# Kernel tuning notes

Hardware: AMD Instinct MI355X
Metric: run time of the kernel (lower is better)

## Reference

```python
import jax, jax.numpy as jnp
import numpy as np

N, H, W, C = 2, 96, 96, 256
HEADS, P = 8, 25
DH = C // HEADS
HID = int(C * 4.0)


def _ln(x, g, b):
    m = jnp.mean(x, axis=-1, keepdims=True)
    v = jnp.var(x, axis=-1, keepdims=True)
    return (x - m) / jnp.sqrt(v + 1e-5) * g + b


def _deform_sample(value, loc, h, w):
    # value: (n, heads, h*w, dh); loc: (n, Lq, heads, P, 2) normalized to [0,1] (x,y)
    # Bilinear sampling with align_corners=False and zero padding, as in
    # grid_sample used by MSDeformAttn.
    n = value.shape[0]
    gx = loc[..., 0] * w - 0.5
    gy = loc[..., 1] * h - 0.5
    x0 = jnp.floor(gx)
    y0 = jnp.floor(gy)
    fx = gx - x0
    fy = gy - y0
    out = jnp.zeros((n, HEADS, gx.shape[1] * P, DH), dtype=value.dtype)
    for dx, dy in ((0, 0), (1, 0), (0, 1), (1, 1)):
        xi = x0 + dx
        yi = y0 + dy
        wgt = (fx if dx else 1.0 - fx) * (fy if dy else 1.0 - fy)
        valid = ((xi >= 0) & (xi <= w - 1) & (yi >= 0) & (yi <= h - 1)).astype(value.dtype)
        xi_c = jnp.clip(xi, 0, w - 1).astype(jnp.int32)
        yi_c = jnp.clip(yi, 0, h - 1).astype(jnp.int32)
        idx = yi_c * w + xi_c                                   # (n, Lq, heads, P)
        idx = jnp.transpose(idx, (0, 2, 1, 3)).reshape(n, HEADS, -1)
        g = jnp.take_along_axis(value, idx[..., None], axis=2)  # (n, heads, Lq*P, dh)
        wv = jnp.transpose(wgt * valid, (0, 2, 1, 3)).reshape(n, HEADS, -1, 1)
        out = out + g * wv
    return out


def setup_inputs() -> dict:
    key = jax.random.key(0)
    ks = jax.random.split(key, 20)
    s = 0.02
    inp = {
        'x': jax.random.normal(ks[0], (N, H, W, C), jnp.float32),
        'ref_points': jax.random.uniform(ks[1], (N, H * W, 1, 2), jnp.float32),
        'spatial_shapes': jnp.array([[H, W]], dtype=jnp.int32),
        'level_start_index': jnp.zeros((1,), dtype=jnp.int32),
        'ln1_g': jnp.ones((C,), jnp.float32),
        'ln1_b': jnp.zeros((C,), jnp.float32),
        'w_off': jax.random.normal(ks[2], (C, HEADS * P * 2), jnp.float32) * s,
        'b_off': jax.random.normal(ks[3], (HEADS * P * 2,), jnp.float32) * s,
        'w_attn': jax.random.normal(ks[4], (C, HEADS * P), jnp.float32) * s,
        'b_attn': jax.random.normal(ks[5], (HEADS * P,), jnp.float32) * s,
        'w_val': jax.random.normal(ks[6], (C, C), jnp.float32) * s,
        'b_val': jnp.zeros((C,), jnp.float32),
        'w_out': jax.random.normal(ks[7], (C, C), jnp.float32) * s,
        'b_out': jnp.zeros((C,), jnp.float32),
        'ln2_g': jnp.ones((C,), jnp.float32),
        'ln2_b': jnp.zeros((C,), jnp.float32),
        'w_fc1': jax.random.normal(ks[8], (C, HID), jnp.float32) * s,
        'b_fc1': jnp.zeros((HID,), jnp.float32),
        'w_fc2': jax.random.normal(ks[9], (HID, C), jnp.float32) * s,
        'b_fc2': jnp.zeros((C,), jnp.float32),
    }
    return inp


def reference(x, ref_points, spatial_shapes, level_start_index,
              ln1_g, ln1_b, w_off, b_off, w_attn, b_attn,
              w_val, b_val, w_out, b_out, ln2_g, ln2_b,
              w_fc1, b_fc1, w_fc2, b_fc2):
    n, h, w, c = x.shape
    lq = h * w
    shortcut = x
    # pre-norm + flatten to query
    q = _ln(x, ln1_g, ln1_b).reshape(n, lq, c)
    # MSDeformAttn (n_levels = 1)
    value = (q @ w_val + b_val).reshape(n, lq, HEADS, DH).transpose(0, 2, 1, 3)
    off = (q @ w_off + b_off).reshape(n, lq, HEADS, P, 2)
    aw = jax.nn.softmax((q @ w_attn + b_attn).reshape(n, lq, HEADS, P), axis=-1)
    norm = jnp.array([w, h], dtype=x.dtype)          # offsets normalized by (W, H)
    ref = ref_points[:, :, 0, :]                     # (n, Lq, 2)
    loc = ref[:, :, None, None, :] + off / norm      # (n, Lq, heads, P, 2)
    sampled = _deform_sample(value, loc, h, w).reshape(n, HEADS, lq, P, DH)
    attn = jnp.einsum('nqhp,nhqpd->nqhd', aw, sampled).reshape(n, lq, c)
    attn = attn @ w_out + b_out
    x1 = shortcut + attn.reshape(n, h, w, c)
    # MLP block
    y = _ln(x1, ln2_g, ln2_b)
    y = jax.nn.gelu(y @ w_fc1 + b_fc1, approximate=False) @ w_fc2 + b_fc2
    return x1 + y
```

## Files before the change

kernel.cpp:

```cpp
#include <hip/hip_runtime.h>
#include <hip/hip_bf16.h>
#include <math.h>

typedef __hip_bfloat16 bf16;
typedef __attribute__((ext_vector_type(8))) short short8;
typedef __attribute__((ext_vector_type(4))) float f32x4;

#define NB 2
#define HH 96
#define WW 96
#define CC 256
#define NHEADS 8
#define PP 25
#define DHH 32
#define HIDN 1024
#define LQ (HH*WW)
#define TT (NB*LQ)
#define NVC 896
#define TB 8

__device__ __forceinline__ float b2f(bf16 v){ return __bfloat162float(v); }
__device__ __forceinline__ bf16  f2b(float v){ return __float2bfloat16(v); }
__device__ __forceinline__ float lo_bf(unsigned u){ return __uint_as_float(u << 16); }
__device__ __forceinline__ float hi_bf(unsigned u){ return __uint_as_float(u & 0xffff0000u); }

__device__ __forceinline__ void gl2lds16(const void* g, void* l) {
    __builtin_amdgcn_global_load_lds(
        (const __attribute__((address_space(1))) unsigned int*)g,
        (__attribute__((address_space(3))) unsigned int*)l, 16, 0, 0);
}

__global__ __launch_bounds__(256) void prep_all(const float* __restrict__ w_val,
                                                const float* __restrict__ w_off,
                                                const float* __restrict__ w_attn,
                                                const float* __restrict__ w_fc1,
                                                const float* __restrict__ w_fc2,
                                                const float* __restrict__ w_out,
                                                const float* __restrict__ b_val,
                                                const float* __restrict__ b_off,
                                                const float* __restrict__ b_attn,
                                                bf16* __restrict__ wvcT,
                                                bf16* __restrict__ wfc1T,
                                                bf16* __restrict__ wfc2T,
                                                bf16* __restrict__ woutT,
                                                float* __restrict__ bvc)
{
    const int idx = blockIdx.x*256 + threadIdx.x;
    if (idx < 229376) {
        int n = idx >> 8, k = idx & 255;
        float v = (n < 256) ? w_val[(size_t)k*256 + n]
                : (n < 656) ? w_off[(size_t)k*400 + (n-256)]
                : (n < 856) ? w_attn[(size_t)k*200 + (n-656)] : 0.f;
        wvcT[idx] = f2b(v);
    } else if (idx < 491520) {
        int j = idx - 229376; int n = j >> 8, k = j & 255;
        wfc1T[j] = f2b(w_fc1[(size_t)k*1024 + n]);
    } else if (idx < 753664) {
        int j = idx - 491520; int n = j >> 10, k = j & 1023;
        wfc2T[j] = f2b(w_fc2[(size_t)k*256 + n]);
    } else if (idx < 819200) {
        int j = idx - 753664; int n = j >> 8, k = j & 255;
        woutT[j] = f2b(w_out[(size_t)k*256 + n]);
    }
    if (idx < NVC)
        bvc[idx] = (idx < 256) ? b_val[idx]
                 : (idx < 656) ? b_off[idx-256]
                 : (idx < 856) ? b_attn[idx-656] : 0.f;
}

__global__ __launch_bounds__(256) void ln_kernel(const float* __restrict__ x,
                                                 const float* __restrict__ g,
                                                 const float* __restrict__ b,
                                                 bf16* __restrict__ out)
{
    const int t = blockIdx.x*4 + (threadIdx.x >> 6);
    const int l = threadIdx.x & 63;
    const float4 v = *(const float4*)(x + (size_t)t*CC + l*4);
    float s  = v.x + v.y + v.z + v.w;
    float s2 = v.x*v.x + v.y*v.y + v.z*v.z + v.w*v.w;
    #pragma unroll
    for (int m = 1; m < 64; m <<= 1) { s += __shfl_xor(s, m); s2 += __shfl_xor(s2, m); }
    const float mean = s * (1.f/CC);
    const float var  = s2 * (1.f/CC) - mean*mean;
    const float rs   = 1.f / sqrtf(var + 1e-5f);
    const float4 gg = *(const float4*)(g + l*4);
    const float4 bb = *(const float4*)(b + l*4);
    bf16 o[4];
    o[0] = f2b((v.x-mean)*rs*gg.x + bb.x);
    o[1] = f2b((v.y-mean)*rs*gg.y + bb.y);
    o[2] = f2b((v.z-mean)*rs*gg.z + bb.z);
    o[3] = f2b((v.w-mean)*rs*gg.w + bb.w);
    *(uint2*)(out + (size_t)t*CC + l*4) = *(uint2*)o;
}

template<int EPI, int K, int N>
__global__ __launch_bounds__(256) void mfma_gemm(const bf16* __restrict__ A,
                                                 const bf16* __restrict__ Bt,
                                                 const float* __restrict__ bias,
                                                 void* __restrict__ outv,
                                                 const float* __restrict__ resid)
{
    __shared__ short As[128*64];
    __shared__ short Bs[128*64];
    const int tid = threadIdx.x;
    const int w = tid >> 6, l = tid & 63;
    const int bm = blockIdx.x, bn = blockIdx.y;

    const bf16* sbase[8];
    short*      lbase[8];
    {
        const int lrow = l >> 3;
        const int q    = (l & 7) ^ lrow;
        #pragma unroll
        for (int j = 0; j < 8; j++) {
            int r = w*8 + j;
            bool isA = r < 16;
            int rr = isA ? r : r - 16;
            int row = rr*8 + lrow;
            size_t grow = (size_t)((isA ? bm : bn)*128 + row);
            sbase[j] = (isA ? A : Bt) + grow*K + q*8;
            lbase[j] = (isA ? As : Bs) + rr*512;
        }
    }

    int aoff[2][4], boff[2][4];
    #pragma unroll
    for (int s = 0; s < 2; s++)
        #pragma unroll
        for (int i = 0; i < 4; i++) {
            int q = s*4 + (l >> 4);
            int m = 64*(w >> 1) + i*16 + (l & 15);
            int n = 64*(w &  1) + i*16 + (l & 15);
            aoff[s][i] = (m*8 + (q ^ (m & 7))) * 8;
            boff[s][i] = (n*8 + (q ^ (n & 7))) * 8;
        }

    f32x4 acc[4][4];
    #pragma unroll
    for (int i = 0; i < 4; i++)
        #pragma unroll
        for (int j = 0; j < 4; j++)
            acc[i][j] = (f32x4){0.f, 0.f, 0.f, 0.f};

    for (int k0 = 0; k0 < K; k0 += 64) {
        #pragma unroll
        for (int j = 0; j < 8; j++)
            gl2lds16(sbase[j] + k0, lbase[j]);
        __syncthreads();
        #pragma unroll
        for (int s = 0; s < 2; s++) {
            short8 af[4], bfr[4];
            #pragma unroll
            for (int i = 0; i < 4; i++) {
                af[i]  = *(const short8*)(As + aoff[s][i]);
                bfr[i] = *(const short8*)(Bs + boff[s][i]);
            }
            #pragma unroll
            for (int i = 0; i < 4; i++)
                #pragma unroll
                for (int j = 0; j < 4; j++)
                    acc[i][j] = __builtin_amdgcn_mfma_f32_16x16x32_bf16(af[i], bfr[j], acc[i][j], 0, 0, 0);
        }
        __syncthreads();
    }

    const int row0 = bm*128 + 64*(w >> 1) + (l >> 4)*4;
    const int col0 = bn*128 + 64*(w &  1) + (l & 15);
    #pragma unroll
    for (int i = 0; i < 4; i++) {
        #pragma unroll
        for (int j = 0; j < 4; j++) {
            const int col = col0 + j*16;
            const float bs = bias[col];
            #pragma unroll
            for (int r = 0; r < 4; r++) {
                const int row = row0 + i*16 + r;
                float v = acc[i][j][r] + bs;
                size_t o = (size_t)row * N + col;
                if (EPI == 0) {
                    ((bf16*)outv)[o] = f2b(v);
                } else if (EPI == 2) {
                    ((bf16*)outv)[o] = f2b(0.5f * v * (1.f + erff(v * 0.70710678118654752f)));
                } else {
                    ((float*)outv)[o] = v + resid[o];
                }
            }
        }
    }
}

struct __align__(16) Tap { _Float16 w[4]; unsigned short i[4]; };

__global__ __launch_bounds__(256) void sample_kernel(const bf16* __restrict__ vc,
                                                     const float* __restrict__ refp,
                                                     bf16* __restrict__ samp)
{
    __shared__ Tap taps[TB*200];
    const int b = blockIdx.x;
    const int tbase = ((b & 7)*288 + (b >> 3)) * TB;
    const int tid = threadIdx.x;

    {
        const int pair = tid >> 2;
        const int j    = tid & 3;
        const int tl   = pair >> 3;
        const int h    = pair & 7;
        const int t    = tbase + tl;
        const bf16* row = vc + (size_t)t*NVC;

        float lg[7];
        #pragma unroll
        for (int k = 0; k < 7; k++) {
            int p = j + 4*k;
            lg[k] = (p < PP) ? b2f(row[656 + h*25 + p]) : -1e30f;
        }
        float m = lg[0];
        #pragma unroll
        for (int k = 1; k < 7; k++) m = fmaxf(m, lg[k]);
        m = fmaxf(m, __shfl_xor(m, 1));
        m = fmaxf(m, __shfl_xor(m, 2));
        float s = 0.f;
        float ex[7];
        #pragma unroll
        for (int k = 0; k < 7; k++) {
            ex[k] = (j + 4*k < PP) ? expf(lg[k] - m) : 0.f;
            s += ex[k];
        }
        s += __shfl_xor(s, 1);
        s += __shfl_xor(s, 2);
        const float inv = 1.f / s;

        const float rx96 = refp[(size_t)t*2 + 0]*96.f - 0.5f;
        const float ry96 = refp[(size_t)t*2 + 1]*96.f - 0.5f;
        const unsigned* offp = (const unsigned*)(row + 256 + h*50);

        #pragma unroll
        for (int k = 0; k < 7; k++) {
            const int p = j + 4*k;
            if (p >= PP) break;
            const float a = ex[k] * inv;
            const unsigned uo = offp[p];
            const float gx = rx96 + lo_bf(uo);
            const float gy = ry96 + hi_bf(uo);
            const float x0f = floorf(gx), y0f = floorf(gy);
            const float fx = gx - x0f, fy = gy - y0f;
            const int ix = (int)x0f, iy = (int)y0f;
            Tap tp;
            #pragma unroll
            for (int d = 0; d < 4; d++) {
                const int dx = d & 1, dy = d >> 1;
                const int xi = ix + dx, yi = iy + dy;
                const bool valid = (xi >= 0) & (xi <= WW-1) & (yi >= 0) & (yi <= HH-1);
                const int xc = min(max(xi, 0), WW-1);
                const int yc = min(max(yi, 0), HH-1);
                tp.i[d] = (unsigned short)(yc*WW + xc);
                tp.w[d] = (_Float16)(valid ? a * (dx ? fx : 1.f-fx) * (dy ? fy : 1.f-fy) : 0.f);
            }
            taps[tl*200 + h*25 + p] = tp;
        }
    }
    __syncthreads();

    const int wv_ = tid >> 6, l = tid & 63;
    const int tl  = wv_*2 + (l >> 5);
    const int r   = l & 31;
    const int h   = r >> 2, oct = r & 3;
    const int c0  = h*DHH + oct*8;
    const int t   = tbase + tl;
    const int n   = (t >= LQ) ? 1 : 0;
    const bf16* pv = vc + (size_t)n*LQ*NVC + c0;
    const int pib = tl*200 + h*25;

    float acc[8] = {0.f,0.f,0.f,0.f,0.f,0.f,0.f,0.f};
    for (int p = 0; p < PP; p++) {
        const uint4 tv = *((const uint4*)taps + (pib + p));
        const _Float16* wp_ = (const _Float16*)&tv;
        const unsigned short* ip_ = (const unsigned short*)&tv + 4;
        #pragma unroll
        for (int d = 0; d < 4; d++) {
            const float wt = (float)wp_[d];
            const uint4 vv = *(const uint4*)(pv + (size_t)ip_[d]*NVC);
            acc[0] += wt*lo_bf(vv.x); acc[1] += wt*hi_bf(vv.x);
            acc[2] += wt*lo_bf(vv.y); acc[3] += wt*hi_bf(vv.y);
            acc[4] += wt*lo_bf(vv.z); acc[5] += wt*hi_bf(vv.z);
            acc[6] += wt*lo_bf(vv.w); acc[7] += wt*hi_bf(vv.w);
        }
    }
    bf16 o[8];
    #pragma unroll
    for (int j2 = 0; j2 < 8; j2++) o[j2] = f2b(acc[j2]);
    *(uint4*)(samp + (size_t)t*CC + c0) = *(uint4*)o;
}

extern "C" void kernel_launch(void* const* d_in, const int* in_sizes, int n_in,
                              void* d_out, int out_size, void* d_ws, size_t ws_size,
                              hipStream_t stream)
{
    const float* x      = (const float*)d_in[0];
    const float* refp   = (const float*)d_in[1];
    const float* ln1_g  = (const float*)d_in[4];
    const float* ln1_b  = (const float*)d_in[5];
    const float* w_off  = (const float*)d_in[6];
    const float* b_off  = (const float*)d_in[7];
    const float* w_attn = (const float*)d_in[8];
    const float* b_attn = (const float*)d_in[9];
    const float* w_val  = (const float*)d_in[10];
    const float* b_val  = (const float*)d_in[11];
    const float* w_out  = (const float*)d_in[12];
    const float* b_out  = (const float*)d_in[13];
    const float* ln2_g  = (const float*)d_in[14];
    const float* ln2_b  = (const float*)d_in[15];
    const float* w_fc1  = (const float*)d_in[16];
    const float* b_fc1  = (const float*)d_in[17];
    const float* w_fc2  = (const float*)d_in[18];
    const float* b_fc2  = (const float*)d_in[19];

    char* wsb = (char*)d_ws;
    bf16*  q     = (bf16*)(wsb + 0);
    bf16*  vc    = (bf16*)(wsb + 9437184);
    bf16*  samp  = (bf16*)(wsb + 42467328);
    float* x1    = (float*)(wsb + 51904512);
    bf16*  wvcT  = (bf16*)(wsb + 70778880);
    bf16*  wfc1T = (bf16*)(wsb + 71237632);
    bf16*  wfc2T = (bf16*)(wsb + 71761920);
    bf16*  woutT = (bf16*)(wsb + 72286208);
    float* bvc   = (float*)(wsb + 72417280);
    bf16*  hid   = (bf16*)(wsb + 0);
    bf16*  y0    = samp;

    if (ws_size < 72420864) return;

    const dim3 blk(256);
    prep_all<<<dim3(3200), blk, 0, stream>>>(w_val, w_off, w_attn, w_fc1, w_fc2, w_out,
                                             b_val, b_off, b_attn,
                                             wvcT, wfc1T, wfc2T, woutT, bvc);
    ln_kernel<<<dim3(TT/4), blk, 0, stream>>>(x, ln1_g, ln1_b, q);
    mfma_gemm<0,256,NVC><<<dim3(TT/128, NVC/128), blk, 0, stream>>>(q, wvcT, bvc, (void*)vc, nullptr);
    sample_kernel<<<dim3(TT/TB), blk, 0, stream>>>(vc, refp, samp);
    mfma_gemm<3,256,CC><<<dim3(TT/128, CC/128), blk, 0, stream>>>(samp, woutT, b_out, (void*)x1, x);
    ln_kernel<<<dim3(TT/4), blk, 0, stream>>>(x1, ln2_g, ln2_b, y0);
    mfma_gemm<2,256,HIDN><<<dim3(TT/128, HIDN/128), blk, 0, stream>>>(y0, wfc1T, b_fc1, (void*)hid, nullptr);
    mfma_gemm<3,HIDN,CC><<<dim3(TT/128, CC/128), blk, 0, stream>>>(hid, wfc2T, b_fc2, d_out, x1);
}
```

Baseline: 249.5 us.

## Add 64-row GEMM tiles for N=256 GEMMs and store value in fp32 compact buffer

Templates the MFMA GEMM on the M tile size so the two GEMMs with N=256 output use 64-row tiles, doubling their block count to fill more CUs. Separately, the value projection epilogue now writes the value columns to a compact fp32 buffer with a 256 stride, and the sampling kernel gathers from it instead of the wide 896-stride bf16 buffer. This is meant to improve locality of the gather, at the cost of twice the bytes per tap and an extra workspace allocation.

```diff
diff --git a/kernel.cpp b/kernel.cpp
--- a/kernel.cpp
+++ b/kernel.cpp
@@ -93,83 +93,94 @@
     *(uint2*)(out + (size_t)t*CC + l*4) = *(uint2*)o;
 }
 
-template<int EPI, int K, int N>
+template<int EPI, int K, int N, int TM>
 __global__ __launch_bounds__(256) void mfma_gemm(const bf16* __restrict__ A,
                                                  const bf16* __restrict__ Bt,
                                                  const float* __restrict__ bias,
                                                  void* __restrict__ outv,
-                                                 const float* __restrict__ resid)
-{
-    __shared__ short As[128*64];
+                                                 const float* __restrict__ resid,
+                                                 float* __restrict__ val32)
+{
+    constexpr int AR  = TM/8;
+    constexpr int TR  = AR + 16;
+    constexpr int RPW = TR/4;
+    constexpr int NJ  = (TM==128) ? 4 : 2;
+    __shared__ short As[TM*64];
     __shared__ short Bs[128*64];
     const int tid = threadIdx.x;
     const int w = tid >> 6, l = tid & 63;
     const int bm = blockIdx.x, bn = blockIdx.y;
 
-    const bf16* sbase[8];
-    short*      lbase[8];
+    const bf16* sbase[RPW];
+    short*      lbase[RPW];
     {
         const int lrow = l >> 3;
         const int q    = (l & 7) ^ lrow;
         #pragma unroll
-        for (int j = 0; j < 8; j++) {
-            int r = w*8 + j;
-            bool isA = r < 16;
-            int rr = isA ? r : r - 16;
+        for (int j = 0; j < RPW; j++) {
+            int r = w*RPW + j;
+            bool isA = r < AR;
+            int rr = isA ? r : r - AR;
             int row = rr*8 + lrow;
-            size_t grow = (size_t)((isA ? bm : bn)*128 + row);
+            size_t grow = (size_t)(isA ? (bm*TM + row) : (bn*128 + row));
             sbase[j] = (isA ? A : Bt) + grow*K + q*8;
             lbase[j] = (isA ? As : Bs) + rr*512;
         }
     }
 
-    int aoff[2][4], boff[2][4];
-    #pragma unroll
-    for (int s = 0; s < 2; s++)
+    const int mbase = (TM==128) ? 64*(w >> 1) : 0;
+    const int nbase = (TM==128) ? 64*(w & 1)  : 32*w;
+
+    int aoff[2][4], boff[2][NJ];
+    #pragma unroll
+    for (int s = 0; s < 2; s++) {
+        const int q = s*4 + (l >> 4);
         #pragma unroll
         for (int i = 0; i < 4; i++) {
-            int q = s*4 + (l >> 4);
-            int m = 64*(w >> 1) + i*16 + (l & 15);
-            int n = 64*(w &  1) + i*16 + (l & 15);
+            int m = mbase + i*16 + (l & 15);
             aoff[s][i] = (m*8 + (q ^ (m & 7))) * 8;
-            boff[s][i] = (n*8 + (q ^ (n & 7))) * 8;
-        }
-
-    f32x4 acc[4][4];
+        }
+        #pragma unroll
+        for (int j = 0; j < NJ; j++) {
+            int n = nbase + j*16 + (l & 15);
+            boff[s][j] = (n*8 + (q ^ (n & 7))) * 8;
+        }
+    }
+
+    f32x4 acc[4][NJ];
     #pragma unroll
     for (int i = 0; i < 4; i++)
         #pragma unroll
-        for (int j = 0; j < 4; j++)
+        for (int j = 0; j < NJ; j++)
             acc[i][j] = (f32x4){0.f, 0.f, 0.f, 0.f};
 
     for (int k0 = 0; k0 < K; k0 += 64) {
         #pragma unroll
-        for (int j = 0; j < 8; j++)
+        for (int j = 0; j < RPW; j++)
             gl2lds16(sbase[j] + k0, lbase[j]);
         __syncthreads();
         #pragma unroll
         for (int s = 0; s < 2; s++) {
-            short8 af[4], bfr[4];
-            #pragma unroll
-            for (int i = 0; i < 4; i++) {
-                af[i]  = *(const short8*)(As + aoff[s][i]);
-                bfr[i] = *(const short8*)(Bs + boff[s][i]);
-            }
+            short8 af[4], bfr[NJ];
+            #pragma unroll
+            for (int i = 0; i < 4; i++)  af[i]  = *(const short8*)(As + aoff[s][i]);
+            #pragma unroll
+            for (int j = 0; j < NJ; j++) bfr[j] = *(const short8*)(Bs + boff[s][j]);
             #pragma unroll
             for (int i = 0; i < 4; i++)
                 #pragma unroll
-                for (int j = 0; j < 4; j++)
+                for (int j = 0; j < NJ; j++)
                     acc[i][j] = __builtin_amdgcn_mfma_f32_16x16x32_bf16(af[i], bfr[j], acc[i][j], 0, 0, 0);
         }
         __syncthreads();
     }
 
-    const int row0 = bm*128 + 64*(w >> 1) + (l >> 4)*4;
-    const int col0 = bn*128 + 64*(w &  1) + (l & 15);
+    const int row0 = bm*TM + mbase + (l >> 4)*4;
+    const int col0 = bn*128 + nbase + (l & 15);
     #pragma unroll
     for (int i = 0; i < 4; i++) {
         #pragma unroll
-        for (int j = 0; j < 4; j++) {
+        for (int j = 0; j < NJ; j++) {
             const int col = col0 + j*16;
             const float bs = bias[col];
             #pragma unroll
@@ -181,8 +192,11 @@
                     ((bf16*)outv)[o] = f2b(v);
                 } else if (EPI == 2) {
                     ((bf16*)outv)[o] = f2b(0.5f * v * (1.f + erff(v * 0.70710678118654752f)));
+                } else if (EPI == 3) {
+                    ((float*)outv)[o] = v + resid[o];
                 } else {
-                    ((float*)outv)[o] = v + resid[o];
+                    if (col < 256) val32[(size_t)row*CC + col] = v;
+                    else           ((bf16*)outv)[o] = f2b(v);
                 }
             }
         }
@@ -192,6 +206,7 @@
 struct __align__(16) Tap { _Float16 w[4]; unsigned short i[4]; };
 
 __global__ __launch_bounds__(256) void sample_kernel(const bf16* __restrict__ vc,
+                                                     const float* __restrict__ val32,
                                                      const float* __restrict__ refp,
                                                      bf16* __restrict__ samp)
 {
@@ -268,7 +283,7 @@
     const int c0  = h*DHH + oct*8;
     const int t   = tbase + tl;
     const int n   = (t >= LQ) ? 1 : 0;
-    const bf16* pv = vc + (size_t)n*LQ*NVC + c0;
+    const float* pv = val32 + (size_t)n*LQ*CC + c0;
     const int pib = tl*200 + h*25;
 
     float acc[8] = {0.f,0.f,0.f,0.f,0.f,0.f,0.f,0.f};
@@ -279,11 +294,13 @@
         #pragma unroll
         for (int d = 0; d < 4; d++) {
             const float wt = (float)wp_[d];
-            const uint4 vv = *(const uint4*)(pv + (size_t)ip_[d]*NVC);
-            acc[0] += wt*lo_bf(vv.x); acc[1] += wt*hi_bf(vv.x);
-            acc[2] += wt*lo_bf(vv.y); acc[3] += wt*hi_bf(vv.y);
-            acc[4] += wt*lo_bf(vv.z); acc[5] += wt*hi_bf(vv.z);
-            acc[6] += wt*lo_bf(vv.w); acc[7] += wt*hi_bf(vv.w);
+            const float* vp = pv + (size_t)ip_[d]*CC;
+            const float4 v0 = *(const float4*)(vp);
+            const float4 v1 = *(const float4*)(vp + 4);
+            acc[0] += wt*v0.x; acc[1] += wt*v0.y;
+            acc[2] += wt*v0.z; acc[3] += wt*v0.w;
+            acc[4] += wt*v1.x; acc[5] += wt*v1.y;
+            acc[6] += wt*v1.z; acc[7] += wt*v1.w;
         }
     }
     bf16 o[8];
@@ -325,20 +342,21 @@
     bf16*  wfc2T = (bf16*)(wsb + 71761920);
     bf16*  woutT = (bf16*)(wsb + 72286208);
     float* bvc   = (float*)(wsb + 72417280);
+    float* val32 = (float*)(wsb + 72420864);
     bf16*  hid   = (bf16*)(wsb + 0);
     bf16*  y0    = samp;
 
-    if (ws_size < 72420864) return;
+    if (ws_size < 91295232) return;
 
     const dim3 blk(256);
     prep_all<<<dim3(3200), blk, 0, stream>>>(w_val, w_off, w_attn, w_fc1, w_fc2, w_out,
                                              b_val, b_off, b_attn,
                                              wvcT, wfc1T, wfc2T, woutT, bvc);
     ln_kernel<<<dim3(TT/4), blk, 0, stream>>>(x, ln1_g, ln1_b, q);
-    mfma_gemm<0,256,NVC><<<dim3(TT/128, NVC/128), blk, 0, stream>>>(q, wvcT, bvc, (void*)vc, nullptr);
-    sample_kernel<<<dim3(TT/TB), blk, 0, stream>>>(vc, refp, samp);
-    mfma_gemm<3,256,CC><<<dim3(TT/128, CC/128), blk, 0, stream>>>(samp, woutT, b_out, (void*)x1, x);
+    mfma_gemm<4,256,NVC,128><<<dim3(TT/128, NVC/128), blk, 0, stream>>>(q, wvcT, bvc, (void*)vc, nullptr, val32);
+    sample_kernel<<<dim3(TT/TB), blk, 0, stream>>>(vc, val32, refp, samp);
+    mfma_gemm<3,256,CC,64><<<dim3(TT/64, CC/128), blk, 0, stream>>>(samp, woutT, b_out, (void*)x1, x, nullptr);
     ln_kernel<<<dim3(TT/4), blk, 0, stream>>>(x1, ln2_g, ln2_b, y0);
-    mfma_gemm<2,256,HIDN><<<dim3(TT/128, HIDN/128), blk, 0, stream>>>(y0, wfc1T, b_fc1, (void*)hid, nullptr);
-    mfma_gemm<3,HIDN,CC><<<dim3(TT/128, CC/128), blk, 0, stream>>>(hid, wfc2T, b_fc2, d_out, x1);
-}
+    mfma_gemm<2,256,HIDN,128><<<dim3(TT/128, HIDN/128), blk, 0, stream>>>(y0, wfc1T, b_fc1, (void*)hid, nullptr, nullptr);
+    mfma_gemm<3,HIDN,CC,64><<<dim3(TT/64, CC/128), blk, 0, stream>>>(hid, wfc2T, b_fc2, d_out, x1, nullptr);
+}
```

New measurement: 275.8 us. 10.5% more time.
